# Kernel optimization log

Hardware: AMD Instinct MI355X
Metric: run time of the kernel (lower is better)

The kernel has to match this reference:

```python
import jax, jax.numpy as jnp
import numpy as np

B, C, H, W = 8, 512, 64, 64
R = 16
CQK = C // R  # 32


def setup_inputs() -> dict:
    key = jax.random.key(0)
    kx, kq, kk, kv = jax.random.split(key, 4)
    x = jax.random.normal(kx, (B, C, H, W), dtype=jnp.float32)
    # Conv1d with kernel_size=1, bias=False == matmul over channel dim
    Wq = jax.random.normal(kq, (CQK, C), dtype=jnp.float32) * (1.0 / np.sqrt(C))
    Wk = jax.random.normal(kk, (CQK, C), dtype=jnp.float32) * (1.0 / np.sqrt(C))
    Wv = jax.random.normal(kv, (C, C), dtype=jnp.float32) * (1.0 / np.sqrt(C))
    return {"x": x, "Wq": Wq, "Wk": Wk, "Wv": Wv}


def reference(x, Wq, Wk, Wv):
    b, c, h, w = x.shape
    xf = x.reshape(b, c, h * w)                 # [b, c, n]
    q = jnp.einsum('dc,bcn->bdn', Wq, xf)       # [b, c/r, n]
    k = jnp.einsum('dc,bcn->bdn', Wk, xf)       # [b, c/r, n]
    attn = jax.nn.softmax(jnp.einsum('bdm,bdn->bmn', q, k), axis=-1)  # [b, n, n]
    v = jnp.einsum('dc,bcn->bdn', Wv, xf)       # [b, c, n]
    out = jnp.einsum('bcm,bmn->bcn', v, attn)   # [b, c, n]
    return out.reshape(b, c, h, w)
```

## Files before the change

### kernel.cpp

```cpp
#include <hip/hip_runtime.h>
#include <hip/hip_bf16.h>


typedef __attribute__((ext_vector_type(8))) short s16x8;
typedef __attribute__((ext_vector_type(4))) float f32x4;

#define MFMA16(a, b, c) __builtin_amdgcn_mfma_f32_16x16x32_bf16((a), (b), (c), 0, 0, 0)

__device__ __forceinline__ ushort f2bf(float f) {
  union { float f; unsigned u; } v; v.f = f;
  return (ushort)((v.u + 0x8000u) >> 16);
}
__device__ __forceinline__ unsigned pack_bf16(float lo, float hi) {
  union { float f; unsigned u; } a, b; a.f = lo; b.f = hi;
  return __builtin_amdgcn_perm(b.u + 0x8000u, a.u + 0x8000u, 0x07060302u);
}
__device__ __forceinline__ float fexp2(float x) { return __builtin_amdgcn_exp2f(x); }

__global__ void k_cvt_w(const float* __restrict__ Wq, const float* __restrict__ Wk,
                        const float* __restrict__ Wv, ushort* __restrict__ Wqb,
                        ushort* __restrict__ Wkb, ushort* __restrict__ Wvb) {
  int i = blockIdx.x * 256 + threadIdx.x;
  if (i < 262144) Wvb[i] = f2bf(Wv[i]);
  else if (i < 278528) Wqb[i - 262144] = f2bf(Wq[i - 262144] * 1.4426950408889634f);
  else if (i < 294912) Wkb[i - 278528] = f2bf(Wk[i - 278528]);
}

__global__ __launch_bounds__(256) void k_xpose(const float* __restrict__ x,
                                               ushort* __restrict__ xT) {
  const int b = blockIdx.z, c0 = blockIdx.y * 64, n0 = blockIdx.x * 256;
  __shared__ uint U[2][64][65];
  const int t = threadIdx.x;
  const int wv = t >> 6, ln = t & 63;
  const float* xp = x + ((size_t)b * 512 + c0 + wv * 16) * 4096 + n0 + ln * 4;
#pragma unroll
  for (int i = 0; i < 16; ++i) {
    float4 f = *(const float4*)(xp + (size_t)i * 4096);
    U[0][wv * 16 + i][ln] = pack_bf16(f.x, f.y);
    U[1][wv * 16 + i][ln] = pack_bf16(f.z, f.w);
  }
  __syncthreads();
  const int c_seg = (t & 7) * 8;
#pragma unroll
  for (int pass = 0; pass < 8; ++pass) {
    const int nl = pass * 32 + (t >> 3);
    const int p = nl >> 1;
    const int h = p & 1, idx = p >> 1;
    const uint sel = (nl & 1) ? 0x07060302u : 0x05040100u;
    uint o[4];
#pragma unroll
    for (int j = 0; j < 4; ++j) {
      uint ua = U[h][c_seg + 2 * j][idx];
      uint ub = U[h][c_seg + 2 * j + 1][idx];
      o[j] = __builtin_amdgcn_perm(ub, ua, sel);
    }
    *(uint4*)(xT + ((size_t)b * 4096 + n0 + nl) * 512 + c0 + c_seg) = *(uint4*)o;
  }
}

__global__ __launch_bounds__(256, 2) void k_proj(const ushort* __restrict__ xT,
                                                 const ushort* __restrict__ Wqb,
                                                 const ushort* __restrict__ Wkb,
                                                 const ushort* __restrict__ Wvb,
                                                 ushort* __restrict__ qb,
                                                 ushort* __restrict__ kb,
                                                 ushort* __restrict__ vb) {
  const int b = blockIdx.y, n0 = blockIdx.x * 64;
  const int lane = threadIdx.x & 63, w = threadIdx.x >> 6;
  const int quad = lane >> 4, l15 = lane & 15;
  const ushort* xT_b = xT + (size_t)b * 4096 * 512;

  const ushort* Wqk = (w < 2) ? (Wqb + (size_t)(w * 16 + l15) * 512)
                              : (Wkb + (size_t)((w - 2) * 16 + l15) * 512);

  f32x4 accv[8][4], accqk[4];
#pragma unroll
  for (int i = 0; i < 8; ++i)
#pragma unroll
    for (int nt = 0; nt < 4; ++nt) accv[i][nt] = {0.f, 0.f, 0.f, 0.f};
#pragma unroll
  for (int nt = 0; nt < 4; ++nt) accqk[nt] = {0.f, 0.f, 0.f, 0.f};

  for (int k0 = 0; k0 < 512; k0 += 32) {
    s16x8 bx[4];
#pragma unroll
    for (int nt = 0; nt < 4; ++nt)
      bx[nt] = *(const s16x8*)(xT_b + (size_t)(n0 + nt * 16 + l15) * 512 + k0 + quad * 8);
#pragma unroll
    for (int i = 0; i < 8; ++i) {
      s16x8 av = *(const s16x8*)(Wvb + (size_t)((8 * w + i) * 16 + l15) * 512 + k0 + quad * 8);
#pragma unroll
      for (int nt = 0; nt < 4; ++nt) accv[i][nt] = MFMA16(av, bx[nt], accv[i][nt]);
    }
    s16x8 aqk = *(const s16x8*)(Wqk + k0 + quad * 8);
#pragma unroll
    for (int nt = 0; nt < 4; ++nt) accqk[nt] = MFMA16(aqk, bx[nt], accqk[nt]);
  }

  ushort* vb_b = vb + (size_t)b * 512 * 4096;
#pragma unroll
  for (int i = 0; i < 8; ++i)
#pragma unroll
    for (int nt = 0; nt < 4; ++nt)
#pragma unroll
      for (int r = 0; r < 4; ++r)
        vb_b[(size_t)((8 * w + i) * 16 + quad * 4 + r) * 4096 + n0 + nt * 16 + l15] =
            f2bf(accv[i][nt][r]);

  ushort* qk_out = (w < 2) ? (qb + (size_t)b * 4096 * 32) : (kb + (size_t)b * 4096 * 32);
#pragma unroll
  for (int nt = 0; nt < 4; ++nt) {
    ushort4 u;
    u.x = f2bf(accqk[nt][0]); u.y = f2bf(accqk[nt][1]);
    u.z = f2bf(accqk[nt][2]); u.w = f2bf(accqk[nt][3]);
    *(ushort4*)(qk_out + (size_t)(n0 + nt * 16 + l15) * 32 + (w & 1) * 16 + quad * 4) = u;
  }
}

__global__ __launch_bounds__(256) void k_pass1(const ushort* __restrict__ qb,
                                               const ushort* __restrict__ kb,
                                               float* __restrict__ Lneg) {
  const int b = blockIdx.y, mt = blockIdx.x;
  const int lane = threadIdx.x & 63, w = threadIdx.x >> 6;
  const int quad = lane >> 4, l15 = lane & 15;
  const int m = mt * 64 + w * 16;
  const ushort* qb_b = qb + (size_t)b * 4096 * 32;
  const ushort* kb_b = kb + (size_t)b * 4096 * 32;
  const s16x8 aqf = *(const s16x8*)(qb_b + (size_t)(m + l15) * 32 + quad * 8);
  float ps[4] = {0.f, 0.f, 0.f, 0.f};
  const f32x4 zf = {0.f, 0.f, 0.f, 0.f};
  for (int n0 = 0; n0 < 4096; n0 += 64) {
#pragma unroll
    for (int nt = 0; nt < 4; ++nt) {
      s16x8 bk = *(const s16x8*)(kb_b + (size_t)(n0 + nt * 16 + l15) * 32 + quad * 8);
      f32x4 s = MFMA16(aqf, bk, zf);
#pragma unroll
      for (int r = 0; r < 4; ++r) ps[r] += fexp2(s[r]);
    }
  }
  for (int off = 1; off < 16; off <<= 1)
#pragma unroll
    for (int r = 0; r < 4; ++r) ps[r] += __shfl_xor(ps[r], off, 64);
  if (l15 == 0)
#pragma unroll
    for (int r = 0; r < 4; ++r)
      Lneg[(size_t)b * 4096 + m + quad * 4 + r] = -log2f(ps[r]);
}

__global__ __launch_bounds__(512, 2) void k_pass2(const ushort* __restrict__ qb,
                                                  const ushort* __restrict__ kb,
                                                  const ushort* __restrict__ vb,
                                                  const float* __restrict__ Lneg,
                                                  float* __restrict__ out) {
  const int blk = blockIdx.x;
  const int b = blk & 7, ntb = blk >> 3;
  const int nbase = ntb * 128;
  const int lane = threadIdx.x & 63, w = threadIdx.x >> 6;
  const int quad = lane >> 4, l15 = lane & 15;
  const int cbase = w * 64;
  const int swz = l15 & 7;
  const int Mw = w >> 1;
  const int Tb = (w & 1) * 4;

  __shared__ __align__(16) ushort PT[2][128 * 64];

  const ushort* qb_b = qb + (size_t)b * 4096 * 32;
  const ushort* kb_b = kb + (size_t)b * 4096 * 32;
  const ushort* vb_b = vb + (size_t)b * 512 * 4096;
  const float* L_b = Lneg + (size_t)b * 4096;

  s16x8 kf[4];
#pragma unroll
  for (int i = 0; i < 4; ++i)
    kf[i] = *(const s16x8*)(kb_b + (size_t)(nbase + (Tb + i) * 16 + l15) * 32 + quad * 8);

  f32x4 acc[4][8];
#pragma unroll
  for (int ci = 0; ci < 4; ++ci)
#pragma unroll
    for (int nt = 0; nt < 8; ++nt) acc[ci][nt] = {0.f, 0.f, 0.f, 0.f};

  s16x8 aqp;
  float4 l4p;
  s16x8 va[4][2];

  auto loadQ = [&](int chunk) {
    const int m0 = chunk * 64;
    aqp = *(const s16x8*)(qb_b + (size_t)(m0 + Mw * 16 + l15) * 32 + quad * 8);
    l4p = *(const float4*)(L_b + m0 + Mw * 16 + quad * 4);
  };
  auto loadV = [&](int chunk) {
    const int m0 = chunk * 64;
#pragma unroll
    for (int ci = 0; ci < 4; ++ci) {
      const ushort* vrow = vb_b + (size_t)(cbase + ci * 16 + l15) * 4096 + m0;
      va[ci][0] = *(const s16x8*)(vrow + quad * 8);
      va[ci][1] = *(const s16x8*)(vrow + 32 + quad * 8);
    }
  };
  auto produce_tile = [&](int buf, int i) {
    char* Pw = (char*)&PT[buf][0];
    const int T = Tb + i;
    f32x4 cin; cin.x = l4p.x; cin.y = l4p.y; cin.z = l4p.z; cin.w = l4p.w;
    f32x4 s = MFMA16(aqp, kf[i], cin);
    uint2 u;
    u.x = pack_bf16(fexp2(s.x), fexp2(s.y));
    u.y = pack_bf16(fexp2(s.z), fexp2(s.w));
    const int row = T * 16 + l15;
    const int gran = (2 * Mw + (quad >> 1)) ^ swz;
    *(uint2*)(Pw + row * 128 + gran * 16 + (quad & 1) * 8) = u;
  };

  loadQ(0);
#pragma unroll
  for (int i = 0; i < 4; ++i) produce_tile(0, i);
  loadQ(1);
  loadV(0);

  for (int chunk = 0; chunk < 64; ++chunk) {
    const int buf = chunk & 1;
    __syncthreads();
    const char* P = (const char*)&PT[buf][0];
    s16x8 p0[4], p1[4];
#pragma unroll
    for (int nt = 0; nt < 4; ++nt) {
      const int row = nt * 16 + l15;
      p0[nt] = *(const s16x8*)(P + row * 128 + (quad ^ swz) * 16);
      p1[nt] = *(const s16x8*)(P + row * 128 + ((4 + quad) ^ swz) * 16);
    }
#pragma unroll
    for (int nt = 0; nt < 4; ++nt) {
#pragma unroll
      for (int ci = 0; ci < 4; ++ci) {
        acc[ci][nt] = MFMA16(va[ci][0], p0[nt], acc[ci][nt]);
        acc[ci][nt] = MFMA16(va[ci][1], p1[nt], acc[ci][nt]);
      }
      if (nt < 2) produce_tile(buf ^ 1, nt);
    }
    s16x8 r0[4], r1[4];
#pragma unroll
    for (int nt = 0; nt < 4; ++nt) {
      const int row = (nt + 4) * 16 + l15;
      r0[nt] = *(const s16x8*)(P + row * 128 + (quad ^ swz) * 16);
      r1[nt] = *(const s16x8*)(P + row * 128 + ((4 + quad) ^ swz) * 16);
    }
#pragma unroll
    for (int nt = 0; nt < 4; ++nt) {
#pragma unroll
      for (int ci = 0; ci < 4; ++ci) {
        acc[ci][nt + 4] = MFMA16(va[ci][0], r0[nt], acc[ci][nt + 4]);
        acc[ci][nt + 4] = MFMA16(va[ci][1], r1[nt], acc[ci][nt + 4]);
      }
      if (nt < 2) produce_tile(buf ^ 1, nt + 2);
    }
    if (chunk < 62) loadQ(chunk + 2);
    if (chunk < 63) loadV(chunk + 1);
  }

  float* out_b = out + (size_t)b * 512 * 4096;
#pragma unroll
  for (int ci = 0; ci < 4; ++ci)
#pragma unroll
    for (int nt = 0; nt < 8; ++nt) {
      const int n = nbase + nt * 16 + l15;
      const int c0 = cbase + ci * 16 + quad * 4;
#pragma unroll
      for (int r = 0; r < 4; ++r) out_b[(size_t)(c0 + r) * 4096 + n] = acc[ci][nt][r];
    }
}

extern "C" void kernel_launch(void* const* d_in, const int* in_sizes, int n_in,
                              void* d_out, int out_size, void* d_ws, size_t ws_size,
                              hipStream_t stream) {
  const float* x  = (const float*)d_in[0];
  const float* Wq = (const float*)d_in[1];
  const float* Wk = (const float*)d_in[2];
  const float* Wv = (const float*)d_in[3];
  float* out = (float*)d_out;

  char* ws = (char*)d_ws;
  ushort* vb  = (ushort*)(ws + 0);
  ushort* xT  = (ushort*)(ws + 33554432);
  ushort* qb  = (ushort*)(ws + 67108864);
  ushort* kb  = (ushort*)(ws + 69206016);
  ushort* Wvb = (ushort*)(ws + 71303168);
  ushort* Wqb = (ushort*)(ws + 71827456);
  ushort* Wkb = (ushort*)(ws + 71860224);
  float*  Lrs = (float*)(ws + 71892992);

  hipLaunchKernelGGL(k_cvt_w, dim3(1152), dim3(256), 0, stream, Wq, Wk, Wv, Wqb, Wkb, Wvb);
  hipLaunchKernelGGL(k_xpose, dim3(16, 8, 8), dim3(256), 0, stream, x, xT);
  hipLaunchKernelGGL(k_proj, dim3(64, 8), dim3(256), 0, stream, xT, Wqb, Wkb, Wvb, qb, kb, vb);
  hipLaunchKernelGGL(k_pass1, dim3(64, 8), dim3(256), 0, stream, qb, kb, Lrs);
  hipLaunchKernelGGL(k_pass2, dim3(256), dim3(512), 0, stream, qb, kb, vb, Lrs, out);
}
```

Measured before the change: 363.3 us.

## Prefetch x tiles in projection loop and reorder PV loop into k-halves

In the projection kernel, the next k-slice of x is loaded into registers before the current slice's MFMAs run, so global load latency is hidden behind compute. In the attention kernel, the V operand is split into two k-halves that are reloaded separately. The chunk loop now produces all next-chunk P tiles up front, then issues the first-half MFMAs while loading the second-half P fragments, and issues V reloads between the halves. The aim is to overlap LDS and global loads with MFMA work, at the cost of more live registers and possibly lower occupancy.

Measured after the change: 366.8 us. No clear change (+1.0%).

```diff
diff --git a/kernel.cpp b/kernel.cpp
--- a/kernel.cpp
+++ b/kernel.cpp
@@ -81,11 +81,16 @@
 #pragma unroll
   for (int nt = 0; nt < 4; ++nt) accqk[nt] = {0.f, 0.f, 0.f, 0.f};
 
+  s16x8 bx[4], bxn[4];
+#pragma unroll
+  for (int nt = 0; nt < 4; ++nt)
+    bx[nt] = *(const s16x8*)(xT_b + (size_t)(n0 + nt * 16 + l15) * 512 + quad * 8);
+
   for (int k0 = 0; k0 < 512; k0 += 32) {
-    s16x8 bx[4];
+    const int kn = (k0 + 32) & 511;
 #pragma unroll
     for (int nt = 0; nt < 4; ++nt)
-      bx[nt] = *(const s16x8*)(xT_b + (size_t)(n0 + nt * 16 + l15) * 512 + k0 + quad * 8);
+      bxn[nt] = *(const s16x8*)(xT_b + (size_t)(n0 + nt * 16 + l15) * 512 + kn + quad * 8);
 #pragma unroll
     for (int i = 0; i < 8; ++i) {
       s16x8 av = *(const s16x8*)(Wvb + (size_t)((8 * w + i) * 16 + l15) * 512 + k0 + quad * 8);
@@ -95,6 +100,8 @@
     s16x8 aqk = *(const s16x8*)(Wqk + k0 + quad * 8);
 #pragma unroll
     for (int nt = 0; nt < 4; ++nt) accqk[nt] = MFMA16(aqk, bx[nt], accqk[nt]);
+#pragma unroll
+    for (int nt = 0; nt < 4; ++nt) bx[nt] = bxn[nt];
   }
 
   ushort* vb_b = vb + (size_t)b * 512 * 4096;
@@ -182,21 +189,24 @@
 
   s16x8 aqp;
   float4 l4p;
-  s16x8 va[4][2];
+  s16x8 va0[4], va1[4];
 
   auto loadQ = [&](int chunk) {
     const int m0 = chunk * 64;
     aqp = *(const s16x8*)(qb_b + (size_t)(m0 + Mw * 16 + l15) * 32 + quad * 8);
     l4p = *(const float4*)(L_b + m0 + Mw * 16 + quad * 4);
   };
-  auto loadV = [&](int chunk) {
+  auto loadV0 = [&](int chunk) {
     const int m0 = chunk * 64;
 #pragma unroll
-    for (int ci = 0; ci < 4; ++ci) {
-      const ushort* vrow = vb_b + (size_t)(cbase + ci * 16 + l15) * 4096 + m0;
-      va[ci][0] = *(const s16x8*)(vrow + quad * 8);
-      va[ci][1] = *(const s16x8*)(vrow + 32 + quad * 8);
-    }
+    for (int ci = 0; ci < 4; ++ci)
+      va0[ci] = *(const s16x8*)(vb_b + (size_t)(cbase + ci * 16 + l15) * 4096 + m0 + quad * 8);
+  };
+  auto loadV1 = [&](int chunk) {
+    const int m0 = chunk * 64;
+#pragma unroll
+    for (int ci = 0; ci < 4; ++ci)
+      va1[ci] = *(const s16x8*)(vb_b + (size_t)(cbase + ci * 16 + l15) * 4096 + m0 + 32 + quad * 8);
   };
   auto produce_tile = [&](int buf, int i) {
     char* Pw = (char*)&PT[buf][0];
@@ -215,46 +225,33 @@
 #pragma unroll
   for (int i = 0; i < 4; ++i) produce_tile(0, i);
   loadQ(1);
-  loadV(0);
+  loadV0(0);
+  loadV1(0);
 
   for (int chunk = 0; chunk < 64; ++chunk) {
     const int buf = chunk & 1;
     __syncthreads();
     const char* P = (const char*)&PT[buf][0];
-    s16x8 p0[4], p1[4];
-#pragma unroll
-    for (int nt = 0; nt < 4; ++nt) {
-      const int row = nt * 16 + l15;
-      p0[nt] = *(const s16x8*)(P + row * 128 + (quad ^ swz) * 16);
-      p1[nt] = *(const s16x8*)(P + row * 128 + ((4 + quad) ^ swz) * 16);
-    }
-#pragma unroll
-    for (int nt = 0; nt < 4; ++nt) {
-#pragma unroll
-      for (int ci = 0; ci < 4; ++ci) {
-        acc[ci][nt] = MFMA16(va[ci][0], p0[nt], acc[ci][nt]);
-        acc[ci][nt] = MFMA16(va[ci][1], p1[nt], acc[ci][nt]);
-      }
-      if (nt < 2) produce_tile(buf ^ 1, nt);
-    }
-    s16x8 r0[4], r1[4];
-#pragma unroll
-    for (int nt = 0; nt < 4; ++nt) {
-      const int row = (nt + 4) * 16 + l15;
-      r0[nt] = *(const s16x8*)(P + row * 128 + (quad ^ swz) * 16);
-      r1[nt] = *(const s16x8*)(P + row * 128 + ((4 + quad) ^ swz) * 16);
-    }
-#pragma unroll
-    for (int nt = 0; nt < 4; ++nt) {
-#pragma unroll
-      for (int ci = 0; ci < 4; ++ci) {
-        acc[ci][nt + 4] = MFMA16(va[ci][0], r0[nt], acc[ci][nt + 4]);
-        acc[ci][nt + 4] = MFMA16(va[ci][1], r1[nt], acc[ci][nt + 4]);
-      }
-      if (nt < 2) produce_tile(buf ^ 1, nt + 2);
-    }
+    s16x8 pg[8];
+#pragma unroll
+    for (int nt = 0; nt < 8; ++nt)
+      pg[nt] = *(const s16x8*)(P + (nt * 16 + l15) * 128 + (quad ^ swz) * 16);
+#pragma unroll
+    for (int i = 0; i < 4; ++i) produce_tile(buf ^ 1, i);
     if (chunk < 62) loadQ(chunk + 2);
-    if (chunk < 63) loadV(chunk + 1);
+    s16x8 rr[8];
+#pragma unroll
+    for (int nt = 0; nt < 8; ++nt) {
+#pragma unroll
+      for (int ci = 0; ci < 4; ++ci) acc[ci][nt] = MFMA16(va0[ci], pg[nt], acc[ci][nt]);
+      rr[nt] = *(const s16x8*)(P + (nt * 16 + l15) * 128 + ((4 + quad) ^ swz) * 16);
+    }
+    if (chunk < 63) loadV0(chunk + 1);
+#pragma unroll
+    for (int nt = 0; nt < 8; ++nt)
+#pragma unroll
+      for (int ci = 0; ci < 4; ++ci) acc[ci][nt] = MFMA16(va1[ci], rr[nt], acc[ci][nt]);
+    if (chunk < 63) loadV1(chunk + 1);
   }
 
   float* out_b = out + (size_t)b * 512 * 4096;
```
